# Kernel optimization log

Measured on AMD Instinct MI355X. Metric: run time of the kernel, lower is better.

## Reference

```python
import jax, jax.numpy as jnp
import numpy as np

HEADS = 8
NEG_SLOPE = 0.2


def _layer_norm(x, g, b, eps=1e-5):
    mu = x.mean(-1, keepdims=True)
    var = ((x - mu) ** 2).mean(-1, keepdims=True)
    return (x - mu) / jnp.sqrt(var + eps) * g + b


def setup_inputs() -> dict:
    key = jax.random.key(0)
    ks = jax.random.split(key, 24)
    N, E, H, L = 512, 260000, 256, 4
    s = 0.05
    return dict(
        x=jax.random.normal(ks[0], (N, 1), jnp.float32),
        edge_index=jax.random.randint(ks[1], (2, E), 0, N),
        edge_attr=jax.random.uniform(ks[2], (E, 3), jnp.float32),
        emb_W=jax.random.normal(ks[3], (1, H)) * s,
        emb_b=jnp.zeros((H,)),
        Wl=jax.random.normal(ks[4], (L, H, H)) * s,
        bl=jnp.zeros((L, H)),
        Wr=jax.random.normal(ks[5], (L, H, H)) * s,
        br=jnp.zeros((L, H)),
        We=jax.random.normal(ks[6], (L, 3, H)) * s,
        att=jax.random.normal(ks[7], (L, HEADS, H // HEADS)) * s,
        gb=jnp.zeros((L, H)),
        ln_g=jnp.ones((L, H)),
        ln_b=jnp.zeros((L, H)),
        p1_W=jax.random.normal(ks[8], (2 * H, H)) * s,
        p1_b=jnp.zeros((H,)),
        p2_W=jax.random.normal(ks[9], (H, H // 2)) * s,
        p2_b=jnp.zeros((H // 2,)),
        p3_W=jax.random.normal(ks[10], (H // 2, 1)) * s,
        p3_b=jnp.zeros((1,)),
        v1_W=jax.random.normal(ks[11], (2 * H, H)) * s,
        v1_b=jnp.zeros((H,)),
        v2_W=jax.random.normal(ks[12], (H, 1)) * s,
        v2_b=jnp.zeros((1,)),
        coupling=jnp.asarray(1.0, jnp.float32),
    )


def reference(x, edge_index, edge_attr, emb_W, emb_b, Wl, bl, Wr, br, We, att,
              gb, ln_g, ln_b, p1_W, p1_b, p2_W, p2_b, p3_W, p3_b,
              v1_W, v1_b, v2_W, v2_b, coupling):
    N = x.shape[0]
    E = edge_attr.shape[0]
    L = Wl.shape[0]
    C = Wl.shape[-1] // HEADS
    src, dst = edge_index[0], edge_index[1]

    # PyG GATv2Conv adds self-loops with edge_attr fill_value='mean'
    # (mean of incoming edge_attr per destination node).
    sums = jax.ops.segment_sum(edge_attr, dst, num_segments=N)
    cnt = jax.ops.segment_sum(jnp.ones((E,), edge_attr.dtype), dst, num_segments=N)
    self_attr = sums / jnp.maximum(cnt, 1.0)[:, None]
    loop = jnp.arange(N)
    src_f = jnp.concatenate([src, loop])            # [E+N]
    dst_f = jnp.concatenate([dst, loop])
    ea_f = jnp.concatenate([edge_attr, self_attr])  # [E+N, 3]

    h = x @ emb_W + emb_b                           # [N, H]
    for l in range(L):
        res = h
        xl = (h @ Wl[l] + bl[l]).reshape(N, HEADS, C)
        xr = (h @ Wr[l] + br[l]).reshape(N, HEADS, C)
        ee = (ea_f @ We[l]).reshape(-1, HEADS, C)
        # GATv2 scoring: leaky_relu(x_l[src]+x_r[dst]+edge) . att
        m = jax.nn.leaky_relu(xl[src_f] + xr[dst_f] + ee, NEG_SLOPE)
        alpha = jnp.einsum('ehc,hc->eh', m, att[l])
        amax = jax.ops.segment_max(alpha, dst_f, num_segments=N)
        alpha = jnp.exp(alpha - amax[dst_f])
        denom = jax.ops.segment_sum(alpha, dst_f, num_segments=N)
        alpha = alpha / denom[dst_f]
        out = jax.ops.segment_sum(xl[src_f] * alpha[..., None], dst_f,
                                  num_segments=N).reshape(N, HEADS * C) + gb[l]
        h = jax.nn.relu(_layer_norm(out + res, ln_g[l], ln_b[l]))

    # graph-level representation (single graph, batch=None branch)
    graph_repr = jnp.concatenate([h.mean(0, keepdims=True),
                                  h.max(0, keepdims=True)], axis=1)  # [1, 2H]

    # all-pairs edge representations (i < j)
    iu, ju = jnp.triu_indices(N, k=1)
    er = jnp.concatenate([h[iu], h[ju]], axis=1)    # [N(N-1)/2, 2H]
    p = jax.nn.relu(er @ p1_W + p1_b)
    p = jax.nn.relu(p @ p2_W + p2_b)
    policy_logits = (p @ p3_W + p3_b).squeeze(-1)   # [N(N-1)/2]

    v = jax.nn.relu(graph_repr @ v1_W + v1_b)
    value = (v @ v2_W + v2_b).squeeze(-1)           # [1]

    # Potts energy: per-color degree-squared approximation of triangles
    colors = jnp.argmax(edge_attr, axis=1)
    energy = jnp.asarray(0.0, h.dtype)
    for c in (1, 2):
        w = (colors == c).astype(h.dtype)
        deg = (jax.ops.segment_sum(w, src, num_segments=N)
               + jax.ops.segment_sum(w, dst, num_segments=N))
        energy = energy + (deg ** 2).sum() / (2.0 * N)
    energy = energy * coupling

    return policy_logits, value, energy
```

## Files before the change

kernel.cpp:

```cpp
#include <hip/hip_runtime.h>
#include <math.h>

#define HDIM 256
#define NHEADS 8
#define NEG 0.2f
#define NB 64
#define SEG 4

typedef float f32x4 __attribute__((ext_vector_type(4)));
typedef _Float16 f16x8 __attribute__((ext_vector_type(8)));
typedef __fp16 fp16v2 __attribute__((ext_vector_type(2)));

__global__ __launch_bounds__(256) void edge_part(
    const int* __restrict__ ei, const float* __restrict__ ea, int E, int CH,
    int* __restrict__ pcnt, float* __restrict__ psum, int* __restrict__ pcol) {
  __shared__ int   lcnt[512];
  __shared__ float ls0[512], ls1[512], ls2[512];
  __shared__ int   lcol[1024];
  int t = threadIdx.x, b = blockIdx.x;
  for (int n = t; n < 512; n += 256) {
    lcnt[n] = 0; ls0[n] = 0.f; ls1[n] = 0.f; ls2[n] = 0.f;
    lcol[n] = 0; lcol[512 + n] = 0;
  }
  __syncthreads();
  int e0 = b * CH, e1 = min(E, e0 + CH);
  for (int e = e0 + t; e < e1; e += 256) {
    int src = ei[e], dst = ei[E + e];
    float a0 = ea[3*e], a1 = ea[3*e+1], a2 = ea[3*e+2];
    atomicAdd(&lcnt[dst], 1);
    atomicAdd(&ls0[dst], a0);
    atomicAdd(&ls1[dst], a1);
    atomicAdd(&ls2[dst], a2);
    int idx = 0; float best = a0;
    if (a1 > best) { best = a1; idx = 1; }
    if (a2 > best) { idx = 2; }
    if (idx) {
      int o = (idx - 1) << 9;
      atomicAdd(&lcol[o + src], 1);
      atomicAdd(&lcol[o + dst], 1);
    }
  }
  __syncthreads();
  for (int n = t; n < 512; n += 256) {
    pcnt[b*512 + n] = lcnt[n];
    psum[(size_t)(0*NB + b)*512 + n] = ls0[n];
    psum[(size_t)(1*NB + b)*512 + n] = ls1[n];
    psum[(size_t)(2*NB + b)*512 + n] = ls2[n];
    pcol[(size_t)(0*NB + b)*512 + n] = lcol[n];
    pcol[(size_t)(1*NB + b)*512 + n] = lcol[512 + n];
  }
}

__global__ __launch_bounds__(256) void red_kernel(
    const int* __restrict__ pcnt, const float* __restrict__ psum,
    const int* __restrict__ pcol,
    int* __restrict__ cnt, float* __restrict__ sred, int* __restrict__ dred,
    int* __restrict__ pbase) {
  int q = blockIdx.x >> 1;
  int n = (blockIdx.x & 1)*256 + threadIdx.x;
  if (q == 0) {
    int run = 0;
#pragma unroll 8
    for (int b = 0; b < NB; ++b) {
      int v = pcnt[b*512 + n];
      pbase[b*512 + n] = run;
      run += v;
    }
    cnt[n] = run;
  } else if (q <= 3) {
    int qq = q - 1;
    float s = 0.f;
#pragma unroll 8
    for (int b = 0; b < NB; ++b) s += psum[(size_t)(qq*NB + b)*512 + n];
    sred[qq*512 + n] = s;
  } else {
    int qq = q - 4;
    int s = 0;
#pragma unroll 8
    for (int b = 0; b < NB; ++b) s += pcol[(size_t)(qq*NB + b)*512 + n];
    dred[qq*512 + n] = s;
  }
}

__global__ __launch_bounds__(512) void scan2(
    const int* __restrict__ cnt, const float* __restrict__ sred,
    const int* __restrict__ dred, int N,
    int* __restrict__ rowp, float4* __restrict__ csr,
    const float* __restrict__ coupling, float* __restrict__ eout) {
  int t = threadIdx.x;
  int c = (t < N) ? cnt[t] : 0;
  __shared__ int sbuf[512];
  int v = (t < N) ? (c + 1) : 0;
  sbuf[t] = v;
  __syncthreads();
  for (int off = 1; off < 512; off <<= 1) {
    int add = (t >= off) ? sbuf[t - off] : 0;
    __syncthreads();
    sbuf[t] += add;
    __syncthreads();
  }
  int incl = sbuf[t], excl = incl - v;
  if (t < N) {
    rowp[t] = excl;
    if (t == N - 1) rowp[N] = incl;
    float inv = 1.f / fmaxf((float)c, 1.f);
    csr[excl] = make_float4(sred[t]*inv, sred[512 + t]*inv, sred[1024 + t]*inv,
                            __int_as_float(t));
  }
  float e = 0.f;
  if (t < N) {
    float d1 = (float)dred[t], d2 = (float)dred[512 + t];
    e = d1*d1 + d2*d2;
  }
#pragma unroll
  for (int off = 1; off < 64; off <<= 1) e += __shfl_xor(e, off);
  __shared__ float wred[8];
  if ((t & 63) == 0) wred[t >> 6] = e;
  __syncthreads();
  if (t == 0) {
    float s = 0.f;
#pragma unroll
    for (int i = 0; i < 8; ++i) s += wred[i];
    eout[0] = coupling[0] * s / (2.f * (float)N);
  }
}

__global__ __launch_bounds__(256) void scatter2(
    const int* __restrict__ ei, const float* __restrict__ ea, int E, int CH,
    const int* __restrict__ rowp, const int* __restrict__ pbase,
    float4* __restrict__ csr) {
  __shared__ int lofs[512];
  int t = threadIdx.x, b = blockIdx.x;
  for (int n = t; n < 512; n += 256) lofs[n] = 0;
  __syncthreads();
  int e0 = b * CH, e1 = min(E, e0 + CH);
  for (int e = e0 + t; e < e1; e += 256) {
    int src = ei[e], dst = ei[E + e];
    float a0 = ea[3*e], a1 = ea[3*e+1], a2 = ea[3*e+2];
    int lp = atomicAdd(&lofs[dst], 1);
    int pos = rowp[dst] + 1 + pbase[b*512 + dst] + lp;
    csr[pos] = make_float4(a0, a1, a2, __int_as_float(src));
  }
}

__global__ __launch_bounds__(256) void emb_kernel(
    const float* __restrict__ x, const float* __restrict__ eW,
    const float* __restrict__ eb, float* __restrict__ h) {
  int n = blockIdx.x, t = threadIdx.x;
  h[n*HDIM + t] = fmaf(x[n], eW[t], eb[t]);
}

__global__ __launch_bounds__(256) void w_prep_all(
    const float* __restrict__ Wl, const float* __restrict__ Wr,
    const float* __restrict__ p1W, unsigned short* __restrict__ dst) {
  int gid = blockIdx.x * 256 + threadIdx.x;
  int s = gid >> 16, e = gid & 65535;
  int k = e >> 8, n = e & 255;
  const float* src = (s < 4) ? (Wl + (size_t)s*65536)
                   : (s < 8) ? (Wr + (size_t)(s-4)*65536)
                             : (p1W + (size_t)(s-8)*65536);
  int c = k >> 5, quad = (k >> 3) & 3, kj = k & 7;
  int nt = n >> 4, nl = n & 15;
  int lane = quad*16 + nl;
  _Float16 hv = (_Float16)src[(size_t)k*256 + n];
  dst[(size_t)s*65536 + ((nt*8 + c)*512 + lane*8 + kj)] = *(unsigned short*)&hv;
}

__global__ __launch_bounds__(256) void dual_gemm_mfma(
    const float* __restrict__ Hm,
    const unsigned short* __restrict__ W1h, const unsigned short* __restrict__ W2h,
    const float* __restrict__ b1, const float* __restrict__ b2,
    float* __restrict__ o1, float* __restrict__ o2) {
  int bx = blockIdx.x, by = blockIdx.y;
  int t = threadIdx.x, w = t >> 6, l = t & 63;
  int quad = l >> 4, nl = l & 15;
  int mt = bx*4 + w;

  const unsigned short* Wh; const float* bias; float* o; int nt;
  if (by < 16) { Wh = W1h; bias = b1; o = o1; nt = by; }
  else         { Wh = W2h; bias = b2; o = o2; nt = by - 16; }

  const float* Ar = Hm + (size_t)(mt*16 + nl)*HDIM + quad*8;
  f32x4 acc = (f32x4){0.f, 0.f, 0.f, 0.f};

#pragma unroll
  for (int c = 0; c < 8; ++c) {
    float4 a0 = *(const float4*)(Ar + c*32);
    float4 a1 = *(const float4*)(Ar + c*32 + 4);
    union { f16x8 v8; fp16v2 v2[4]; } u;
    u.v2[0] = __builtin_amdgcn_cvt_pkrtz(a0.x, a0.y);
    u.v2[1] = __builtin_amdgcn_cvt_pkrtz(a0.z, a0.w);
    u.v2[2] = __builtin_amdgcn_cvt_pkrtz(a1.x, a1.y);
    u.v2[3] = __builtin_amdgcn_cvt_pkrtz(a1.z, a1.w);
    f16x8 bfrag = *(const f16x8*)(Wh + (size_t)((nt*8 + c)*512 + l*8));
    acc = __builtin_amdgcn_mfma_f32_16x16x32_f16(u.v8, bfrag, acc, 0, 0, 0);
  }

  int colg = nt*16 + nl;
  float bv = bias ? bias[colg] : 0.f;
#pragma unroll
  for (int r = 0; r < 4; ++r)
    o[(size_t)(mt*16 + quad*4 + r)*HDIM + colg] = acc[r] + bv;
}

__global__ __launch_bounds__(256) void attn_gather(
    const float* __restrict__ xl, const float* __restrict__ xr,
    const float4* __restrict__ csr, const int* __restrict__ row_start,
    const float* __restrict__ We, const float* __restrict__ att,
    float* __restrict__ pm, float* __restrict__ pl, float* __restrict__ pacc) {
  int nb = blockIdx.x;
  int n = nb >> 2, sgm = nb & (SEG - 1);
  int t = threadIdx.x;
  int g = t >> 5, l = t & 31, hd = l >> 2, qd = l & 3;
  int cb = hd*32 + qd*8;

  float xrv[8], w0[8], w1[8], w2[8], av[8];
#pragma unroll
  for (int j = 0; j < 8; ++j) {
    xrv[j] = xr[(size_t)n*HDIM + cb + j];
    w0[j]  = We[cb + j];
    w1[j]  = We[HDIM + cb + j];
    w2[j]  = We[2*HDIM + cb + j];
    av[j]  = att[cb + j];
  }
  int rs = row_start[n], re = row_start[n+1], len = re - rs;
  int s0 = rs + ((len * sgm) >> 2);
  int s1 = rs + ((len * (sgm + 1)) >> 2);

  float mh = -INFINITY, lh = 0.f;
  float acc[8] = {0.f,0.f,0.f,0.f,0.f,0.f,0.f,0.f};

  int idx = s0 + g;
  if (idx < s1) {
    float4 rec = csr[idx];
    while (idx < s1) {
      int idxn = idx + 8;
      float4 recn = csr[idxn < s1 ? idxn : rs];
      int s = __float_as_int(rec.w);
      const float* xp = xl + (size_t)s*HDIM + cb;
      float xv[8];
      float4 x0 = *(const float4*)xp;
      float4 x1 = *(const float4*)(xp + 4);
      xv[0]=x0.x; xv[1]=x0.y; xv[2]=x0.z; xv[3]=x0.w;
      xv[4]=x1.x; xv[5]=x1.y; xv[6]=x1.z; xv[7]=x1.w;
      float partial = 0.f;
#pragma unroll
      for (int j = 0; j < 8; ++j) {
        float m = fmaf(rec.z, w2[j], fmaf(rec.y, w1[j], fmaf(rec.x, w0[j], xrv[j]))) + xv[j];
        m = fmaxf(m, NEG * m);
        partial = fmaf(m, av[j], partial);
      }
      partial += __shfl_xor(partial, 1);
      partial += __shfl_xor(partial, 2);
      if (partial > mh) {
        float sc = __expf(mh - partial);
        lh *= sc;
#pragma unroll
        for (int j = 0; j < 8; ++j) acc[j] *= sc;
        mh = partial;
      }
      float pw = __expf(partial - mh);
      lh += pw;
#pragma unroll
      for (int j = 0; j < 8; ++j) acc[j] = fmaf(pw, xv[j], acc[j]);
      rec = recn; idx = idxn;
    }
  }

  __shared__ float lacc[8][HDIM];
  __shared__ float lm[8][NHEADS];
  __shared__ float llv[8][NHEADS];
#pragma unroll
  for (int j = 0; j < 8; ++j) lacc[g][cb + j] = acc[j];
  if (qd == 0) { lm[g][hd] = mh; llv[g][hd] = lh; }
  __syncthreads();

  int c = t, hh = c >> 5;
  float M = -INFINITY;
#pragma unroll
  for (int g2 = 0; g2 < 8; ++g2) M = fmaxf(M, lm[g2][hh]);
  float L = 0.f, o = 0.f;
#pragma unroll
  for (int g2 = 0; g2 < 8; ++g2) {
    float e2 = __expf(lm[g2][hh] - M);
    L = fmaf(llv[g2][hh], e2, L);
    o = fmaf(lacc[g2][c], e2, o);
  }
  pacc[(size_t)nb*HDIM + c] = o;
  if ((c & 31) == 0) {
    pm[nb*NHEADS + hh] = M;
    pl[nb*NHEADS + hh] = L;
  }
}

__global__ __launch_bounds__(256) void attn_merge(
    const float* __restrict__ pm, const float* __restrict__ pl,
    const float* __restrict__ pacc,
    const float* __restrict__ gb, const float* __restrict__ lng,
    const float* __restrict__ lnb,
    const float* __restrict__ h_in, float* __restrict__ h_out) {
  int n = blockIdx.x, t = threadIdx.x;
  int c = t, hh = c >> 5;
  float M = -INFINITY;
#pragma unroll
  for (int s = 0; s < SEG; ++s) M = fmaxf(M, pm[(n*SEG + s)*NHEADS + hh]);
  float L = 0.f, o = 0.f;
#pragma unroll
  for (int s = 0; s < SEG; ++s) {
    float e2 = __expf(pm[(n*SEG + s)*NHEADS + hh] - M);
    L = fmaf(pl[(n*SEG + s)*NHEADS + hh], e2, L);
    o = fmaf(pacc[(size_t)(n*SEG + s)*HDIM + c], e2, o);
  }
  float val = o / L + gb[c] + h_in[(size_t)n*HDIM + c];

  float s1 = val, s2 = val * val;
#pragma unroll
  for (int off = 1; off < 64; off <<= 1) {
    s1 += __shfl_xor(s1, off);
    s2 += __shfl_xor(s2, off);
  }
  __shared__ float rs1[4], rs2[4];
  if ((t & 63) == 0) { rs1[t >> 6] = s1; rs2[t >> 6] = s2; }
  __syncthreads();
  float S1 = rs1[0] + rs1[1] + rs1[2] + rs1[3];
  float S2 = rs2[0] + rs2[1] + rs2[2] + rs2[3];
  float mu = S1 * (1.f/HDIM);
  float var = S2 * (1.f/HDIM) - mu * mu;
  float y = (val - mu) * rsqrtf(var + 1e-5f);
  y = fmaf(y, lng[c], lnb[c]);
  h_out[(size_t)n*HDIM + c] = fmaxf(y, 0.f);
}

__global__ __launch_bounds__(256) void w2_prep_kernel(
    const float* __restrict__ W2, unsigned short* __restrict__ W2h) {
  int tid = blockIdx.x * 256 + threadIdx.x;
  int k = tid >> 7, n = tid & 127;
  int c = k >> 5, kq = (k >> 3) & 3, kj = k & 7;
  int nt = n >> 4, nl = n & 15;
  int lane = kq*16 + nl;
  _Float16 hv = (_Float16)W2[(size_t)k*128 + n];
  W2h[(size_t)(((c*8 + nt)*64 + lane)*8 + kj)] = *(unsigned short*)&hv;
}

__global__ __launch_bounds__(256, 4) void pair_mfma_kernel(
    const float* __restrict__ A, const float* __restrict__ Bm,
    const unsigned short* __restrict__ W2h,
    const float* __restrict__ b2, const float* __restrict__ W3,
    const float* __restrict__ b3, float* __restrict__ out, int N) {
  int bb = blockIdx.x;
  int half = bb & 1;
  int b = bb >> 1, ti = 0, rem = 32;
  while (b >= rem) { b -= rem; ti++; rem--; }
  int tj = ti + b;
  int i0 = ti * 16 + half * 8;
  int j0 = tj * 16;

  int t = threadIdx.x;
  int w = t >> 6, l = t & 63;
  int quad = l >> 4, nl = l & 15;

  float b2v[8], w3v[8];
#pragma unroll
  for (int nt = 0; nt < 8; ++nt) {
    b2v[nt] = b2[nt*16 + nl];
    w3v[nt] = W3[nt*16 + nl];
  }

  const float* Brow = Bm + (size_t)(j0 + nl) * HDIM;
  const float* Arow0 = A + (size_t)(i0 + w*2) * HDIM;

  f32x4 acc[2][8];
#pragma unroll
  for (int a2 = 0; a2 < 2; ++a2)
#pragma unroll
    for (int nt = 0; nt < 8; ++nt) acc[a2][nt] = (f32x4){0.f,0.f,0.f,0.f};

  for (int c = 0; c < 8; ++c) {
    int kb = c*32 + quad*8;
    float4 bv0 = *(const float4*)(Brow + kb);
    float4 bv1 = *(const float4*)(Brow + kb + 4);

    f16x8 afrag[2];
#pragma unroll
    for (int a2 = 0; a2 < 2; ++a2) {
      const float* Ar = Arow0 + (size_t)a2*HDIM + kb;
      float4 av0 = *(const float4*)Ar;
      float4 av1 = *(const float4*)(Ar + 4);
      union { f16x8 v8; fp16v2 v2[4]; } u;
      u.v2[0] = __builtin_amdgcn_cvt_pkrtz(fmaxf(av0.x + bv0.x, 0.f),
                                           fmaxf(av0.y + bv0.y, 0.f));
      u.v2[1] = __builtin_amdgcn_cvt_pkrtz(fmaxf(av0.z + bv0.z, 0.f),
                                           fmaxf(av0.w + bv0.w, 0.f));
      u.v2[2] = __builtin_amdgcn_cvt_pkrtz(fmaxf(av1.x + bv1.x, 0.f),
                                           fmaxf(av1.y + bv1.y, 0.f));
      u.v2[3] = __builtin_amdgcn_cvt_pkrtz(fmaxf(av1.z + bv1.z, 0.f),
                                           fmaxf(av1.w + bv1.w, 0.f));
      afrag[a2] = u.v8;
    }

#pragma unroll
    for (int nt = 0; nt < 8; ++nt) {
      f16x8 bfrag = *(const f16x8*)(W2h + (size_t)(((c*8 + nt)*64 + l) * 8));
#pragma unroll
      for (int a2 = 0; a2 < 2; ++a2)
        acc[a2][nt] = __builtin_amdgcn_mfma_f32_16x16x32_f16(
            afrag[a2], bfrag, acc[a2][nt], 0, 0, 0);
    }
  }

  float b3v = b3[0];
#pragma unroll
  for (int a2 = 0; a2 < 2; ++a2) {
    int i = i0 + w*2 + a2;
#pragma unroll
    for (int r = 0; r < 4; ++r) {
      float s = 0.f;
#pragma unroll
      for (int nt = 0; nt < 8; ++nt)
        s = fmaf(fmaxf(acc[a2][nt][r] + b2v[nt], 0.f), w3v[nt], s);
      s += __shfl_xor(s, 1);
      s += __shfl_xor(s, 2);
      s += __shfl_xor(s, 4);
      s += __shfl_xor(s, 8);
      if (nl == 0) {
        int j = j0 + quad*4 + r;
        if (i < j)
          out[(size_t)i*(2*N - i - 1)/2 + (j - i - 1)] = s + b3v;
      }
    }
  }
}

__global__ __launch_bounds__(256) void pool_kernel(
    const float* __restrict__ h, float* __restrict__ psums,
    float* __restrict__ pmaxs) {
  int g = blockIdx.x, t = threadIdx.x;
  float s = 0.f, m = -INFINITY;
#pragma unroll
  for (int r = 0; r < 16; ++r) {
    float v = h[(size_t)(g*16 + r)*HDIM + t];
    s += v; m = fmaxf(m, v);
  }
  psums[g*HDIM + t] = s;
  pmaxs[g*HDIM + t] = m;
}

__global__ __launch_bounds__(256) void value1_kernel(
    const float* __restrict__ psums, const float* __restrict__ pmaxs,
    const float* __restrict__ v1W, float* __restrict__ vpart, int N) {
  int b = blockIdx.x, t = threadIdx.x;
  int k0 = b * 16;
  int kk = t >> 4, g = t & 15;
  __shared__ float repr16[16];
  int k = k0 + kk;
  float v;
  if (k < HDIM) {
    v = psums[g*HDIM + k] + psums[(g + 16)*HDIM + k];
    v += __shfl_xor(v, 1); v += __shfl_xor(v, 2);
    v += __shfl_xor(v, 4); v += __shfl_xor(v, 8);
    if (g == 0) repr16[kk] = v / (float)N;
  } else {
    int kc = k - HDIM;
    v = fmaxf(pmaxs[g*HDIM + kc], pmaxs[(g + 16)*HDIM + kc]);
    v = fmaxf(v, __shfl_xor(v, 1)); v = fmaxf(v, __shfl_xor(v, 2));
    v = fmaxf(v, __shfl_xor(v, 4)); v = fmaxf(v, __shfl_xor(v, 8));
    if (g == 0) repr16[kk] = v;
  }
  __syncthreads();
  float pv = 0.f;
#pragma unroll
  for (int q = 0; q < 16; ++q)
    pv = fmaf(repr16[q], v1W[(size_t)(k0 + q)*HDIM + t], pv);
  vpart[b*HDIM + t] = pv;
}

__global__ __launch_bounds__(256) void value2_kernel(
    const float* __restrict__ vpart, const float* __restrict__ v1b,
    const float* __restrict__ v2W, const float* __restrict__ v2b,
    float* __restrict__ out) {
  int t = threadIdx.x;
  float a = 0.f;
#pragma unroll
  for (int g = 0; g < 32; ++g) a += vpart[g*HDIM + t];
  a = fmaxf(a + v1b[t], 0.f);
  float pv = a * v2W[t];
#pragma unroll
  for (int off = 1; off < 64; off <<= 1) pv += __shfl_xor(pv, off);
  __shared__ float wsum[4];
  if ((t & 63) == 0) wsum[t >> 6] = pv;
  __syncthreads();
  if (t == 0) out[0] = wsum[0] + wsum[1] + wsum[2] + wsum[3] + v2b[0];
}

extern "C" void kernel_launch(void* const* d_in, const int* in_sizes, int n_in,
                              void* d_out, int out_size, void* d_ws, size_t ws_size,
                              hipStream_t stream) {
  const float* x    = (const float*)d_in[0];
  const int*   ei   = (const int*)  d_in[1];
  const float* ea   = (const float*)d_in[2];
  const float* embW = (const float*)d_in[3];
  const float* embb = (const float*)d_in[4];
  const float* Wl   = (const float*)d_in[5];
  const float* bl   = (const float*)d_in[6];
  const float* Wr   = (const float*)d_in[7];
  const float* br   = (const float*)d_in[8];
  const float* We   = (const float*)d_in[9];
  const float* att  = (const float*)d_in[10];
  const float* gb   = (const float*)d_in[11];
  const float* lng  = (const float*)d_in[12];
  const float* lnb  = (const float*)d_in[13];
  const float* p1W  = (const float*)d_in[14];
  const float* p1b  = (const float*)d_in[15];
  const float* p2W  = (const float*)d_in[16];
  const float* p2b  = (const float*)d_in[17];
  const float* p3W  = (const float*)d_in[18];
  const float* p3b  = (const float*)d_in[19];
  const float* v1W  = (const float*)d_in[20];
  const float* v1b  = (const float*)d_in[21];
  const float* v2W  = (const float*)d_in[22];
  const float* v2b  = (const float*)d_in[23];
  const float* coup = (const float*)d_in[24];

  int N = in_sizes[0];
  int E = in_sizes[2] / 3;
  float* out = (float*)d_out;
  size_t P = (size_t)N*(N-1)/2;

  char* w = (char*)d_ws;
  int*    rowp = (int*)   (w + 0);
  float*  plS  = (float*) (w + 2560);
  float*  plM  = (float*) (w + 35328);
  float*  vprt = (float*) (w + 68096);
  float4* csr  = (float4*)(w + 101120);
  size_t csr_end = 101120 + (size_t)(E + N) * 16;
  csr_end = (csr_end + 255) & ~(size_t)255;
  float* hA  = (float*)(w + csr_end);
  float* hB  = hA  + (size_t)N*HDIM;
  float* xlb = hB  + (size_t)N*HDIM;
  float* xrb = xlb + (size_t)N*HDIM;
  float* Ab  = xrb + (size_t)N*HDIM;
  float* Bb  = Ab  + (size_t)N*HDIM;
  unsigned short* W2h   = (unsigned short*)(Bb + (size_t)N*HDIM);
  unsigned short* Whall = W2h + 32768;
  size_t ubase = ((size_t)((char*)(Whall + 10*65536) - w) + 255) & ~(size_t)255;

  char* U = w + ubase;
  int*    pcnt = (int*)   (U + 0);
  float*  psum = (float*) (U + 131072);
  int*    pcol = (int*)   (U + 524288);
  int*    pbase= (int*)   (U + 786432);
  int*    cnt  = (int*)   (U + 917504);
  float*  sred = (float*) (U + 919552);
  int*    dred = (int*)   (U + 925696);
  float*  pmv  = (float*) (U + 0);
  float*  plv  = (float*) (U + 65536);
  float*  pacc = (float*) (U + 131072);

  int CH = (E + NB - 1) / NB;
  edge_part<<<NB, 256, 0, stream>>>(ei, ea, E, CH, pcnt, psum, pcol);
  red_kernel<<<12, 256, 0, stream>>>(pcnt, psum, pcol, cnt, sred, dred, pbase);
  scan2<<<1, 512, 0, stream>>>(cnt, sred, dred, N, rowp, csr, coup, out + P + 1);
  scatter2<<<NB, 256, 0, stream>>>(ei, ea, E, CH, rowp, pbase, csr);
  emb_kernel<<<N, 256, 0, stream>>>(x, embW, embb, hA);
  w2_prep_kernel<<<128, 256, 0, stream>>>(p2W, W2h);
  w_prep_all<<<2560, 256, 0, stream>>>(Wl, Wr, p1W, Whall);

  float* hin = hA;
  float* hout = hB;
  for (int l = 0; l < 4; ++l) {
    dual_gemm_mfma<<<dim3(8, 32), 256, 0, stream>>>(hin,
        Whall + (size_t)l*65536, Whall + (size_t)(4 + l)*65536,
        bl + l*HDIM, br + l*HDIM, xlb, xrb);
    attn_gather<<<N*SEG, 256, 0, stream>>>(xlb, xrb, csr, rowp,
        We + (size_t)l*3*HDIM, att + (size_t)l*HDIM, pmv, plv, pacc);
    attn_merge<<<N, 256, 0, stream>>>(pmv, plv, pacc,
        gb + (size_t)l*HDIM, lng + (size_t)l*HDIM, lnb + (size_t)l*HDIM,
        hin, hout);
    float* tmp = hin; hin = hout; hout = tmp;
  }

  dual_gemm_mfma<<<dim3(8, 32), 256, 0, stream>>>(hin,
      Whall + (size_t)8*65536, Whall + (size_t)9*65536,
      p1b, (const float*)nullptr, Ab, Bb);

  pair_mfma_kernel<<<1056, 256, 0, stream>>>(Ab, Bb, W2h, p2b, p3W, p3b, out, N);

  pool_kernel<<<32, 256, 0, stream>>>(hin, plS, plM);
  value1_kernel<<<32, 256, 0, stream>>>(plS, plM, v1W, vprt, N);
  value2_kernel<<<1, 256, 0, stream>>>(vprt, v1b, v2W, v2b, out + P);
}
```

Measured before the change: 319.5 us.

## Gather source features in fp16 in attention and widen edge partition grid

The dual GEMM now also writes an fp16 copy of the xl projection, and attn_gather reads 16 bytes per edge from that copy instead of 32 bytes of fp32, halving the bytes moved by the gather-heavy attention loop. Separately, the edge partitioning block count rises from 64 to 256 for more parallelism in the preprocessing kernels, and the workspace offsets grow to fit the larger partial buffers. The fp16 rounding of xl adds small numeric error to the attention logits and messages, and the GEMM does extra stores.

```diff
diff --git a/kernel.cpp b/kernel.cpp
--- a/kernel.cpp
+++ b/kernel.cpp
@@ -4,7 +4,7 @@
 #define HDIM 256
 #define NHEADS 8
 #define NEG 0.2f
-#define NB 64
+#define NB 256
 #define SEG 4
 
 typedef float f32x4 __attribute__((ext_vector_type(4)));
@@ -170,15 +170,17 @@
     const float* __restrict__ Hm,
     const unsigned short* __restrict__ W1h, const unsigned short* __restrict__ W2h,
     const float* __restrict__ b1, const float* __restrict__ b2,
-    float* __restrict__ o1, float* __restrict__ o2) {
+    float* __restrict__ o1, float* __restrict__ o2,
+    unsigned short* __restrict__ o1h) {
   int bx = blockIdx.x, by = blockIdx.y;
   int t = threadIdx.x, w = t >> 6, l = t & 63;
   int quad = l >> 4, nl = l & 15;
   int mt = bx*4 + w;
 
   const unsigned short* Wh; const float* bias; float* o; int nt;
-  if (by < 16) { Wh = W1h; bias = b1; o = o1; nt = by; }
-  else         { Wh = W2h; bias = b2; o = o2; nt = by - 16; }
+  bool first = (by < 16);
+  if (first) { Wh = W1h; bias = b1; o = o1; nt = by; }
+  else       { Wh = W2h; bias = b2; o = o2; nt = by - 16; }
 
   const float* Ar = Hm + (size_t)(mt*16 + nl)*HDIM + quad*8;
   f32x4 acc = (f32x4){0.f, 0.f, 0.f, 0.f};
@@ -199,12 +201,19 @@
   int colg = nt*16 + nl;
   float bv = bias ? bias[colg] : 0.f;
 #pragma unroll
-  for (int r = 0; r < 4; ++r)
-    o[(size_t)(mt*16 + quad*4 + r)*HDIM + colg] = acc[r] + bv;
+  for (int r = 0; r < 4; ++r) {
+    float val = acc[r] + bv;
+    size_t idx = (size_t)(mt*16 + quad*4 + r)*HDIM + colg;
+    o[idx] = val;
+    if (first && o1h) {
+      _Float16 hv = (_Float16)val;
+      o1h[idx] = *(unsigned short*)&hv;
+    }
+  }
 }
 
 __global__ __launch_bounds__(256) void attn_gather(
-    const float* __restrict__ xl, const float* __restrict__ xr,
+    const unsigned short* __restrict__ xlh, const float* __restrict__ xr,
     const float4* __restrict__ csr, const int* __restrict__ row_start,
     const float* __restrict__ We, const float* __restrict__ att,
     float* __restrict__ pm, float* __restrict__ pl, float* __restrict__ pacc) {
@@ -237,12 +246,11 @@
       int idxn = idx + 8;
       float4 recn = csr[idxn < s1 ? idxn : rs];
       int s = __float_as_int(rec.w);
-      const float* xp = xl + (size_t)s*HDIM + cb;
+      union { f16x8 v8; _Float16 h[8]; } ux;
+      ux.v8 = *(const f16x8*)(xlh + (size_t)s*HDIM + cb);
       float xv[8];
-      float4 x0 = *(const float4*)xp;
-      float4 x1 = *(const float4*)(xp + 4);
-      xv[0]=x0.x; xv[1]=x0.y; xv[2]=x0.z; xv[3]=x0.w;
-      xv[4]=x1.x; xv[5]=x1.y; xv[6]=x1.z; xv[7]=x1.w;
+#pragma unroll
+      for (int j = 0; j < 8; ++j) xv[j] = (float)ux.h[j];
       float partial = 0.f;
 #pragma unroll
       for (int j = 0; j < 8; ++j) {
@@ -540,18 +548,19 @@
   float* xrb = xlb + (size_t)N*HDIM;
   float* Ab  = xrb + (size_t)N*HDIM;
   float* Bb  = Ab  + (size_t)N*HDIM;
-  unsigned short* W2h   = (unsigned short*)(Bb + (size_t)N*HDIM);
+  unsigned short* xlh   = (unsigned short*)(Bb + (size_t)N*HDIM);
+  unsigned short* W2h   = xlh + (size_t)N*HDIM;
   unsigned short* Whall = W2h + 32768;
   size_t ubase = ((size_t)((char*)(Whall + 10*65536) - w) + 255) & ~(size_t)255;
 
   char* U = w + ubase;
   int*    pcnt = (int*)   (U + 0);
-  float*  psum = (float*) (U + 131072);
-  int*    pcol = (int*)   (U + 524288);
-  int*    pbase= (int*)   (U + 786432);
-  int*    cnt  = (int*)   (U + 917504);
-  float*  sred = (float*) (U + 919552);
-  int*    dred = (int*)   (U + 925696);
+  float*  psum = (float*) (U + 524288);
+  int*    pcol = (int*)   (U + 2097152);
+  int*    pbase= (int*)   (U + 3145728);
+  int*    cnt  = (int*)   (U + 3670016);
+  float*  sred = (float*) (U + 3672064);
+  int*    dred = (int*)   (U + 3678208);
   float*  pmv  = (float*) (U + 0);
   float*  plv  = (float*) (U + 65536);
   float*  pacc = (float*) (U + 131072);
@@ -570,8 +579,8 @@
   for (int l = 0; l < 4; ++l) {
     dual_gemm_mfma<<<dim3(8, 32), 256, 0, stream>>>(hin,
         Whall + (size_t)l*65536, Whall + (size_t)(4 + l)*65536,
-        bl + l*HDIM, br + l*HDIM, xlb, xrb);
-    attn_gather<<<N*SEG, 256, 0, stream>>>(xlb, xrb, csr, rowp,
+        bl + l*HDIM, br + l*HDIM, xlb, xrb, xlh);
+    attn_gather<<<N*SEG, 256, 0, stream>>>(xlh, xrb, csr, rowp,
         We + (size_t)l*3*HDIM, att + (size_t)l*HDIM, pmv, plv, pacc);
     attn_merge<<<N, 256, 0, stream>>>(pmv, plv, pacc,
         gb + (size_t)l*HDIM, lng + (size_t)l*HDIM, lnb + (size_t)l*HDIM,
@@ -581,7 +590,7 @@
 
   dual_gemm_mfma<<<dim3(8, 32), 256, 0, stream>>>(hin,
       Whall + (size_t)8*65536, Whall + (size_t)9*65536,
-      p1b, (const float*)nullptr, Ab, Bb);
+      p1b, (const float*)nullptr, Ab, Bb, (unsigned short*)nullptr);
 
   pair_mfma_kernel<<<1056, 256, 0, stream>>>(Ab, Bb, W2h, p2b, p3W, p3b, out, N);
 
```

Measured after the change: 315.1 us. No clear change (-1.4%).
